# Performance work log

Measured on AMD Instinct MI355X. Metric: run time of the kernel, lower is better.

## Reference

```python
import math
import jax, jax.numpy as jnp
import numpy as np

B, L, D, H = 2, 2048, 1024, 16
HD = D // H  # 64

def setup_inputs() -> dict:
    key = jax.random.key(0)
    k1, k2, k3 = jax.random.split(key, 3)
    x = jax.random.normal(k1, (B, L, D), dtype=jnp.float32)
    Wqkv = jax.random.normal(k2, (3 * D, D), dtype=jnp.float32) * (1.0 / math.sqrt(D))
    Wo = jax.random.normal(k3, (D, D), dtype=jnp.float32) * (1.0 / math.sqrt(D))
    return {"x": x, "Wqkv": Wqkv, "Wo": Wo}

def reference(x, Wqkv, Wo):
    # QKV projection (torch Linear: y = x @ W.T), then split
    qkv = jnp.einsum('bld,ed->ble', x, Wqkv)  # [B, L, 3D]
    q, k, v = jnp.split(qkv, 3, axis=-1)
    # [B, H, L, HD]
    q = q.reshape(B, L, H, HD).transpose(0, 2, 1, 3)
    k = k.reshape(B, L, H, HD).transpose(0, 2, 1, 3)
    v = v.reshape(B, L, H, HD).transpose(0, 2, 1, 3)
    # scores; causal mask applied before the 1/sqrt(d) scale (as in source;
    # -inf is unchanged by scaling so math matches scale-then-mask)
    scores = jnp.einsum('bhqd,bhkd->bhqk', q, k)
    causal = jnp.tril(jnp.ones((L, L), dtype=bool))
    scores = jnp.where(causal, scores, -jnp.inf)
    attn = jax.nn.softmax(scores / math.sqrt(HD), axis=-1)
    out = jnp.einsum('bhqk,bhkd->bhqd', attn, v)  # [B, H, L, HD]
    out = out.transpose(0, 2, 1, 3).reshape(B, L, D)
    # output projection (dropout is identity in eval / p=0)
    return jnp.einsum('bld,ed->ble', out, Wo)
```

## Files before the change

### kernel.cpp

```cpp
#include <hip/hip_runtime.h>
#include <hip/hip_bf16.h>
#include <cstdint>
#include <cstddef>

#define B_SZ 2
#define L_SEQ 2048
#define DM 1024
#define NH 16
#define HDIM 64
#define BL (B_SZ * L_SEQ)
#define QKV_N (3 * DM)

typedef __attribute__((ext_vector_type(4))) float f32x4;
typedef __attribute__((ext_vector_type(16))) float f32x16;
typedef __attribute__((ext_vector_type(8))) short bf16x8;
typedef __attribute__((ext_vector_type(4))) unsigned int u32x4;
typedef unsigned short u16;
typedef __attribute__((ext_vector_type(4))) unsigned short u16x4;

__device__ __forceinline__ float bf2f(u16 u) {
  union { unsigned int i; float f; } c; c.i = ((unsigned int)u) << 16; return c.f;
}
__device__ __forceinline__ u16 f2bf(float f) {
  union { float f; unsigned int i; } c; c.f = f;
  unsigned int r = c.i + 0x7fffu + ((c.i >> 16) & 1u);
  return (u16)(r >> 16);
}

__device__ __forceinline__ void gload_lds16(const void* g, void* l) {
  __builtin_amdgcn_global_load_lds(
      (const __attribute__((address_space(1))) void*)g,
      (__attribute__((address_space(3))) void*)l, 16, 0, 0);
}

__device__ __forceinline__ f32x16 mfma32(bf16x8 a, bf16x8 b, f32x16 c) {
  return __builtin_amdgcn_mfma_f32_32x32x16_bf16(a, b, c, 0, 0, 0);
}

__device__ __forceinline__ unsigned cvtpk(float lo, float hi) {
  unsigned r;
  asm("v_cvt_pk_bf16_f32 %0, %1, %2" : "=v"(r) : "v"(lo), "v"(hi));
  return r;
}
__device__ __forceinline__ void plswap(unsigned& a, unsigned& b) {
  asm("v_permlane32_swap_b32 %0, %1" : "+v"(a), "+v"(b));
}

template <int BASE>
__device__ __forceinline__ bf16x8 pack_bfrag(const f32x16& v) {
  unsigned a  = cvtpk(v[BASE + 0], v[BASE + 1]);
  unsigned a2 = cvtpk(v[BASE + 2], v[BASE + 3]);
  unsigned b  = cvtpk(v[BASE + 4], v[BASE + 5]);
  unsigned b2 = cvtpk(v[BASE + 6], v[BASE + 7]);
  plswap(a, b);
  plswap(a2, b2);
  u32x4 fw; fw[0] = a; fw[1] = a2; fw[2] = b; fw[3] = b2;
  return __builtin_bit_cast(bf16x8, fw);
}

__global__ __launch_bounds__(256) void cvt_f32_bf16(const float* __restrict__ in,
                                                    u16* __restrict__ out, int n4) {
  int i = blockIdx.x * blockDim.x + threadIdx.x;
  const int stride = gridDim.x * blockDim.x;
  for (; i < n4; i += stride) {
    float4 v = ((const float4*)in)[i];
    u16x4 o;
    o[0] = f2bf(v.x); o[1] = f2bf(v.y); o[2] = f2bf(v.z); o[3] = f2bf(v.w);
    ((u16x4*)out)[i] = o;
  }
}

template <bool BF16_OUT>
__global__ __launch_bounds__(256) void gemm_bt(
    const u16* __restrict__ A, const u16* __restrict__ B,
    void* __restrict__ Cv, int M, int N, int K) {
  __shared__ u16 As[128 * 32];
  __shared__ u16 Bs[128 * 32];
  const int tid = threadIdx.x;
  const int lane = tid & 63, w = tid >> 6;
  const int lr = lane & 15, lg = lane >> 4;
  const int wr = w >> 1, wc = w & 1;
  const int bm = blockIdx.y * 128, bn = blockIdx.x * 128;

  f32x4 acc[4][4] = {};

  const int l4 = lane >> 2;
  const int csw = ((lane & 3) ^ ((lane >> 3) & 3)) * 8;
  const size_t aoff0 = (size_t)(bm + (w * 2 + 0) * 16 + l4) * K + csw;
  const size_t aoff1 = (size_t)(bm + (w * 2 + 1) * 16 + l4) * K + csw;
  const size_t boff0 = (size_t)(bn + (w * 2 + 0) * 16 + l4) * K + csw;
  const size_t boff1 = (size_t)(bn + (w * 2 + 1) * 16 + l4) * K + csw;
  u16* As0 = As + (w * 2 + 0) * 512;
  u16* As1 = As + (w * 2 + 1) * 512;
  u16* Bs0 = Bs + (w * 2 + 0) * 512;
  u16* Bs1 = Bs + (w * 2 + 1) * 512;
  const int sw_rd = (lr >> 1) & 3;

  for (int k0 = 0; k0 < K; k0 += 32) {
    gload_lds16(A + aoff0 + k0, As0);
    gload_lds16(A + aoff1 + k0, As1);
    gload_lds16(B + boff0 + k0, Bs0);
    gload_lds16(B + boff1 + k0, Bs1);
    __syncthreads();

    bf16x8 af[4], bfr[4];
#pragma unroll
    for (int mt = 0; mt < 4; ++mt) {
      const int row = wr * 64 + mt * 16 + lr;
      af[mt] = *(const bf16x8*)&As[row * 32 + ((lg ^ sw_rd) * 8)];
    }
#pragma unroll
    for (int nt = 0; nt < 4; ++nt) {
      const int row = wc * 64 + nt * 16 + lr;
      bfr[nt] = *(const bf16x8*)&Bs[row * 32 + ((lg ^ sw_rd) * 8)];
    }
#pragma unroll
    for (int mt = 0; mt < 4; ++mt)
#pragma unroll
      for (int nt = 0; nt < 4; ++nt)
        acc[mt][nt] = __builtin_amdgcn_mfma_f32_16x16x32_bf16(af[mt], bfr[nt],
                                                              acc[mt][nt], 0, 0, 0);
    __syncthreads();
  }

#pragma unroll
  for (int mt = 0; mt < 4; ++mt)
#pragma unroll
    for (int nt = 0; nt < 4; ++nt)
#pragma unroll
      for (int r = 0; r < 4; ++r) {
        const int row = bm + wr * 64 + mt * 16 + lg * 4 + r;
        const int col = bn + wc * 64 + nt * 16 + lr;
        if (BF16_OUT)
          ((u16*)Cv)[(size_t)row * N + col] = f2bf(acc[mt][nt][r]);
        else
          ((float*)Cv)[(size_t)row * N + col] = acc[mt][nt][r];
      }
}

__device__ const uint8_t JQT[24] = {15,14,13,12,11,10,9,8, 7, 15, 14,6, 13,5,
                                    12,4, 11,3, 10,2, 9,1, 8,0};
__device__ const uint8_t JT0[24] = {0,0,0,0,0,0,0,0, 0, 16, 16,0, 16,0,
                                    16,0, 16,0, 16,0, 16,0, 16,0};
__device__ const uint8_t JT1[24] = {16,16,16,16,16,16,16,16, 16, 32, 30,14, 28,12,
                                    26,10, 24,8, 22,6, 20,4, 18,2};

__global__ __launch_bounds__(256) void attn_fused(const u16* __restrict__ qkv,
                                                  u16* __restrict__ aout,
                                                  float* __restrict__ opart,
                                                  float2* __restrict__ mlb) {
  __shared__ u16 Kl[2][64 * 64];
  __shared__ u16 Vt[2][64 * 64];

  const int tid = threadIdx.x;
  const int lane = tid & 63, w = tid >> 6;
  const int l31 = lane & 31, hi = lane >> 5;
  const int id = (int)blockIdx.x;
  const int bh = id & 31, j = id >> 5;
  const int qt = JQT[j];
  const int t0 = JT0[j], t1 = JT1[j];
  const int b = bh >> 4, h = bh & 15;
  const u16* base = qkv + (size_t)b * L_SEQ * QKV_N;
  const int W = qt * 128 + w * 32;
  const int qrow = W + l31;

  const int krow = tid >> 2;
  const int ks0 = (tid & 3) * 2;
  const int kr7 = krow & 7;
  const u16* gpk_base = base + (size_t)krow * QKV_N + DM + h * HDIM + ks0 * 8;
  bf16x8 kr0, kr1;

  const int vd0 = (tid & 31) * 2;
  const int vkb = tid >> 5;
  const int vge = tid & 7;
  const int vgo = (tid & 7) ^ 4;
  const u16* gpv_base = base + (size_t)(vkb * 8) * QKV_N + 2 * DM + h * HDIM + vd0;
  unsigned int vtmp[8];

  auto issue_loads = [&](int t) {
    const u16* gpk = gpk_base + (size_t)t * 64 * QKV_N;
    kr0 = *(const bf16x8*)(gpk);
    kr1 = *(const bf16x8*)(gpk + 8);
    const u16* gpv = gpv_base + (size_t)t * 64 * QKV_N;
#pragma unroll
    for (int jj = 0; jj < 8; ++jj)
      vtmp[jj] = *(const unsigned int*)(gpv + (size_t)jj * QKV_N);
  };
  auto write_lds = [&](int buf) {
    *(bf16x8*)&Kl[buf][krow * 64 + ((ks0 ^ kr7) * 8)] = kr0;
    *(bf16x8*)&Kl[buf][krow * 64 + (((ks0 + 1) ^ kr7) * 8)] = kr1;
    u32x4 lo, hiw;
#pragma unroll
    for (int jj = 0; jj < 4; ++jj) {
      lo[jj]  = __builtin_amdgcn_perm(vtmp[2 * jj + 1], vtmp[2 * jj], 0x05040100u);
      hiw[jj] = __builtin_amdgcn_perm(vtmp[2 * jj + 1], vtmp[2 * jj], 0x07060302u);
    }
    *(u32x4*)&Vt[buf][vd0 * 64 + ((vkb ^ vge) * 8)] = lo;
    *(u32x4*)&Vt[buf][(vd0 + 1) * 64 + ((vkb ^ vgo) * 8)] = hiw;
  };

  bf16x8 bq[4];
  {
    const u16* qp = base + (size_t)qrow * QKV_N + h * HDIM + hi * 8;
#pragma unroll
    for (int dc = 0; dc < 4; ++dc) {
      bf16x8 tq = *(const bf16x8*)(qp + dc * 16);
#pragma unroll
      for (int i = 0; i < 8; ++i)
        tq[i] = (short)f2bf(bf2f((u16)tq[i]) * 0.18033688f);
      bq[dc] = tq;
    }
  }

  f32x16 acc0 = {}, acc1 = {};
  float mrow = -1e30f, lrow = 0.f;

  const int vg = ((l31 >> 1) & 7) ^ ((l31 & 1) << 2);
  const int lsw = l31 & 7;

  issue_loads(t0);
  write_lds(0);
  __syncthreads();

  for (int t = t0; t < t1; ++t) {
    const int cur = (t - t0) & 1;
    if (t + 1 < t1) issue_loads(t + 1);

    if (64 * t <= W + 31) {
      f32x16 s0 = {}, s1 = {};
#pragma unroll
      for (int dc = 0; dc < 4; ++dc) {
        const int sl = ((dc * 2 + hi) ^ lsw) * 8;
        const bf16x8 k0 = *(const bf16x8*)&Kl[cur][l31 * 64 + sl];
        const bf16x8 k1 = *(const bf16x8*)&Kl[cur][(32 + l31) * 64 + sl];
        s0 = mfma32(k0, bq[dc], s0);
        s1 = mfma32(k1, bq[dc], s1);
      }

      if (64 * t + 63 > W) {
#pragma unroll
        for (int r = 0; r < 16; ++r) {
          const int kg = t * 64 + (r & 3) + 8 * (r >> 2) + 4 * hi;
          if (kg > qrow) s0[r] = -1e30f;
          if (kg + 32 > qrow) s1[r] = -1e30f;
        }
      }

      float mx[8];
#pragma unroll
      for (int i = 0; i < 8; ++i)
        mx[i] = fmaxf(fmaxf(s0[i], s0[i + 8]), fmaxf(s1[i], s1[i + 8]));
#pragma unroll
      for (int i = 0; i < 4; ++i) mx[i] = fmaxf(mx[i], mx[i + 4]);
      float px = fmaxf(fmaxf(mx[0], mx[2]), fmaxf(mx[1], mx[3]));
      px = fmaxf(px, __shfl_xor(px, 32));

      if (!__all(px <= mrow + 8.f)) {
        const float mnew = fmaxf(mrow, px);
        const float alpha = exp2f(mrow - mnew);
        mrow = mnew;
        lrow *= alpha;
#pragma unroll
        for (int i = 0; i < 16; ++i) { acc0[i] *= alpha; acc1[i] *= alpha; }
      }

#pragma unroll
      for (int r = 0; r < 16; ++r) {
        s0[r] = exp2f(s0[r] - mrow);
        s1[r] = exp2f(s1[r] - mrow);
      }
      float sm[8];
#pragma unroll
      for (int i = 0; i < 8; ++i)
        sm[i] = (s0[i] + s0[i + 8]) + (s1[i] + s1[i + 8]);
#pragma unroll
      for (int i = 0; i < 4; ++i) sm[i] += sm[i + 4];
      float rs = (sm[0] + sm[2]) + (sm[1] + sm[3]);
      rs += __shfl_xor(rs, 32);
      lrow += rs;

      const bf16x8 pf0 = pack_bfrag<0>(s0);
      const bf16x8 pf1 = pack_bfrag<8>(s0);
      const bf16x8 pf2 = pack_bfrag<0>(s1);
      const bf16x8 pf3 = pack_bfrag<8>(s1);

#pragma unroll
      for (int c = 0; c < 4; ++c) {
        const bf16x8 pf = c == 0 ? pf0 : c == 1 ? pf1 : c == 2 ? pf2 : pf3;
        const int sl = ((c * 2 + hi) ^ vg) * 8;
        const bf16x8 va = *(const bf16x8*)&Vt[cur][l31 * 64 + sl];
        const bf16x8 vb = *(const bf16x8*)&Vt[cur][(32 + l31) * 64 + sl];
        acc0 = mfma32(va, pf, acc0);
        acc1 = mfma32(vb, pf, acc1);
      }
    }

    if (t + 1 < t1) write_lds(((t + 1) - t0) & 1);
    __syncthreads();
  }

  if (qt >= 8) {
    const int c = (t0 == 16) ? 1 : 0;
    const int slot = ((qt - 8) * 2 + c) * 32 + bh;
    float* po = opart + (size_t)slot * 8192 + (w * 32 + l31);
#pragma unroll
    for (int i = 0; i < 16; ++i) {
      const int d0 = (i & 3) + 8 * (i >> 2) + 4 * hi;
      po[d0 * 128] = acc0[i];
      po[(d0 + 32) * 128] = acc1[i];
    }
    if (hi == 0) mlb[slot * 128 + w * 32 + l31] = make_float2(mrow, lrow);
  } else {
    const float inv = 1.f / lrow;
#pragma unroll
    for (int i = 0; i < 16; ++i) { acc0[i] *= inv; acc1[i] *= inv; }
    const bf16x8 of0 = pack_bfrag<0>(acc0);
    const bf16x8 of1 = pack_bfrag<8>(acc0);
    const bf16x8 of2 = pack_bfrag<0>(acc1);
    const bf16x8 of3 = pack_bfrag<8>(acc1);
    u16* op = aout + (size_t)(b * L_SEQ + qrow) * DM + h * HDIM + hi * 8;
    *(bf16x8*)(op + 0)  = of0;
    *(bf16x8*)(op + 16) = of1;
    *(bf16x8*)(op + 32) = of2;
    *(bf16x8*)(op + 48) = of3;
  }
}

__global__ __launch_bounds__(256) void attn_combine(
    const float* __restrict__ opart, const float2* __restrict__ mlb,
    u16* __restrict__ aout) {
  const int gw = ((int)blockIdx.x * 256 + (int)threadIdx.x) >> 6;
  const int lane = threadIdx.x & 63;
  const int u = gw >> 1, qh = gw & 1;
  const int qt = 8 + (u >> 5), bh = u & 31;
  const int b = bh >> 4, h = bh & 15;
  const int s1 = ((qt - 8) * 2) * 32 + bh, s2 = s1 + 32;
  const int q = qh * 64 + lane;
  const float2 ml1 = mlb[s1 * 128 + q];
  const float2 ml2 = mlb[s2 * 128 + q];
  const float m = fmaxf(ml1.x, ml2.x);
  const float a1 = exp2f(ml1.x - m), a2 = exp2f(ml2.x - m);
  const float invl = 1.f / (ml1.y * a1 + ml2.y * a2);
  const float c1 = a1 * invl, c2 = a2 * invl;
  const float* p1 = opart + (size_t)s1 * 8192 + q;
  const float* p2 = opart + (size_t)s2 * 8192 + q;
  const int qrow = qt * 128 + q;
  u16* op = aout + (size_t)(b * L_SEQ + qrow) * DM + h * HDIM;
#pragma unroll
  for (int d0 = 0; d0 < 64; d0 += 8) {
    u16x4 o0, o1;
#pragma unroll
    for (int jj = 0; jj < 4; ++jj) {
      o0[jj] = f2bf(p1[(d0 + jj) * 128] * c1 + p2[(d0 + jj) * 128] * c2);
      o1[jj] = f2bf(p1[(d0 + 4 + jj) * 128] * c1 + p2[(d0 + 4 + jj) * 128] * c2);
    }
    *(u16x4*)(op + d0) = o0;
    *(u16x4*)(op + d0 + 4) = o1;
  }
}

extern "C" void kernel_launch(void* const* d_in, const int* in_sizes, int n_in,
                              void* d_out, int out_size, void* d_ws, size_t ws_size,
                              hipStream_t stream) {
  (void)in_sizes; (void)n_in; (void)out_size; (void)ws_size;
  const float* x = (const float*)d_in[0];
  const float* wqkv = (const float*)d_in[1];
  const float* wo = (const float*)d_in[2];

  char* ws = (char*)d_ws;
  u16* x_bf = (u16*)(ws);
  u16* w_bf = (u16*)(ws + (size_t)(8u << 20));
  u16* wo_bf = (u16*)(ws + (size_t)(14u << 20));
  u16* qkv_bf = (u16*)(ws + (size_t)(16u << 20));
  u16* ao_bf = x_bf;
  float* opart = (float*)d_out;
  float2* mlb = (float2*)(ws + (size_t)(8u << 20));

  cvt_f32_bf16<<<2048, 256, 0, stream>>>(x, x_bf, BL * DM / 4);
  cvt_f32_bf16<<<2048, 256, 0, stream>>>(wqkv, w_bf, QKV_N * DM / 4);
  cvt_f32_bf16<<<1024, 256, 0, stream>>>(wo, wo_bf, DM * DM / 4);

  dim3 g1(QKV_N / 128, BL / 128);
  gemm_bt<true><<<g1, 256, 0, stream>>>(x_bf, w_bf, (void*)qkv_bf, BL, QKV_N, DM);

  attn_fused<<<dim3(768), 256, 0, stream>>>(qkv_bf, ao_bf, opart, mlb);
  attn_combine<<<dim3(128), 256, 0, stream>>>(opart, mlb, ao_bf);

  dim3 g3(DM / 128, BL / 128);
  gemm_bt<false><<<g3, 256, 0, stream>>>(ao_bf, wo_bf, d_out, BL, DM, DM);
}
```

Measured before the change: 138.6 us.

## Split causal attention KV range into finer chunks with bf16 partials

Reworks the causal attention work split so that query tiles 4-15 are divided into KV chunks of 8 tiles (up to 4 chunks per query tile). This grows the grid from 768 to 1280 blocks for better load balance across CUs. Partial outputs are now stored as bf16 instead of fp32, spread over two buffers, to cut partial-result traffic. The combine kernel now merges up to four partials per row. The cost is more combine work, a larger split-KV overhead, and slightly lower precision in the partials.

```diff
diff --git a/kernel.cpp b/kernel.cpp
--- a/kernel.cpp
+++ b/kernel.cpp
@@ -138,16 +138,22 @@
       }
 }
 
-__device__ const uint8_t JQT[24] = {15,14,13,12,11,10,9,8, 7, 15, 14,6, 13,5,
-                                    12,4, 11,3, 10,2, 9,1, 8,0};
-__device__ const uint8_t JT0[24] = {0,0,0,0,0,0,0,0, 0, 16, 16,0, 16,0,
-                                    16,0, 16,0, 16,0, 16,0, 16,0};
-__device__ const uint8_t JT1[24] = {16,16,16,16,16,16,16,16, 16, 32, 30,14, 28,12,
-                                    26,10, 24,8, 22,6, 20,4, 18,2};
+__device__ const uint8_t JQT[40] = {15,15,15,15, 14,14,14, 13,13,13, 12,12,12,
+                                    11,11,11, 10,10, 9,9, 8,8, 7,7, 6, 5, 4, 3,
+                                    14, 10, 6, 2, 13, 9, 5, 1, 12, 8, 4, 0};
+__device__ const uint8_t JT0[40] = {0,8,16,24, 0,8,16, 0,8,16, 0,8,16,
+                                    0,8,16, 0,8, 0,8, 0,8, 0,8, 0, 0, 0, 0,
+                                    24, 16, 8, 0, 24, 16, 8, 0, 24, 16, 8, 0};
+__device__ const uint8_t JT1[40] = {8,16,24,32, 8,16,24, 8,16,24, 8,16,24,
+                                    8,16,24, 8,16, 8,16, 8,16, 8,16, 8, 8, 8, 8,
+                                    30, 22, 14, 6, 28, 20, 12, 4, 26, 18, 10, 2};
+__device__ const uint8_t SBASE[16] = {255,255,255,255, 0,2,4,6,
+                                      8,11,14,17, 20,24,28,32};
 
 __global__ __launch_bounds__(256) void attn_fused(const u16* __restrict__ qkv,
                                                   u16* __restrict__ aout,
-                                                  float* __restrict__ opart,
+                                                  u16* __restrict__ opart_lo,
+                                                  u16* __restrict__ opart_hi,
                                                   float2* __restrict__ mlb) {
   __shared__ u16 Kl[2][64 * 64];
   __shared__ u16 Vt[2][64 * 64];
@@ -299,17 +305,19 @@
     __syncthreads();
   }
 
-  if (qt >= 8) {
-    const int c = (t0 == 16) ? 1 : 0;
-    const int slot = ((qt - 8) * 2 + c) * 32 + bh;
-    float* po = opart + (size_t)slot * 8192 + (w * 32 + l31);
+  if (SBASE[qt] != 255) {
+    const int c = t0 >> 3;
+    const int slot = ((int)SBASE[qt] + c) * 32 + bh;
+    u16* po = slot < 1024 ? opart_lo + (size_t)slot * 8192
+                          : opart_hi + (size_t)(slot - 1024) * 8192;
+    const int q = w * 32 + l31;
 #pragma unroll
     for (int i = 0; i < 16; ++i) {
       const int d0 = (i & 3) + 8 * (i >> 2) + 4 * hi;
-      po[d0 * 128] = acc0[i];
-      po[(d0 + 32) * 128] = acc1[i];
-    }
-    if (hi == 0) mlb[slot * 128 + w * 32 + l31] = make_float2(mrow, lrow);
+      po[d0 * 128 + q] = f2bf(acc0[i]);
+      po[(d0 + 32) * 128 + q] = f2bf(acc1[i]);
+    }
+    if (hi == 0) mlb[slot * 128 + q] = make_float2(mrow, lrow);
   } else {
     const float inv = 1.f / lrow;
 #pragma unroll
@@ -327,35 +335,54 @@
 }
 
 __global__ __launch_bounds__(256) void attn_combine(
-    const float* __restrict__ opart, const float2* __restrict__ mlb,
-    u16* __restrict__ aout) {
-  const int gw = ((int)blockIdx.x * 256 + (int)threadIdx.x) >> 6;
-  const int lane = threadIdx.x & 63;
-  const int u = gw >> 1, qh = gw & 1;
-  const int qt = 8 + (u >> 5), bh = u & 31;
+    const u16* __restrict__ opart_lo, const u16* __restrict__ opart_hi,
+    const float2* __restrict__ mlb, u16* __restrict__ aout) {
+  const int gid = (int)blockIdx.x * 256 + (int)threadIdx.x;
+  const int q = gid & 127;
+  const int u = gid >> 7;
+  const int qt = 4 + (u >> 5), bh = u & 31;
   const int b = bh >> 4, h = bh & 15;
-  const int s1 = ((qt - 8) * 2) * 32 + bh, s2 = s1 + 32;
-  const int q = qh * 64 + lane;
-  const float2 ml1 = mlb[s1 * 128 + q];
-  const float2 ml2 = mlb[s2 * 128 + q];
-  const float m = fmaxf(ml1.x, ml2.x);
-  const float a1 = exp2f(ml1.x - m), a2 = exp2f(ml2.x - m);
-  const float invl = 1.f / (ml1.y * a1 + ml2.y * a2);
-  const float c1 = a1 * invl, c2 = a2 * invl;
-  const float* p1 = opart + (size_t)s1 * 8192 + q;
-  const float* p2 = opart + (size_t)s2 * 8192 + q;
+  const int nc = (2 * qt + 9) >> 3;
+  const int sb = (int)SBASE[qt];
+
+  float2 ml[4];
+  const u16* pp[4];
+  float mm = -1e30f;
+#pragma unroll
+  for (int c = 0; c < 4; ++c)
+    if (c < nc) {
+      const int slot = (sb + c) * 32 + bh;
+      ml[c] = mlb[slot * 128 + q];
+      pp[c] = slot < 1024 ? opart_lo + (size_t)slot * 8192
+                          : opart_hi + (size_t)(slot - 1024) * 8192;
+      mm = fmaxf(mm, ml[c].x);
+    }
+  float L = 0.f, cf[4];
+#pragma unroll
+  for (int c = 0; c < 4; ++c)
+    if (c < nc) { cf[c] = exp2f(ml[c].x - mm); L += ml[c].y * cf[c]; }
+  const float invl = 1.f / L;
+#pragma unroll
+  for (int c = 0; c < 4; ++c)
+    if (c < nc) cf[c] *= invl;
+
   const int qrow = qt * 128 + q;
   u16* op = aout + (size_t)(b * L_SEQ + qrow) * DM + h * HDIM;
 #pragma unroll
   for (int d0 = 0; d0 < 64; d0 += 8) {
-    u16x4 o0, o1;
-#pragma unroll
-    for (int jj = 0; jj < 4; ++jj) {
-      o0[jj] = f2bf(p1[(d0 + jj) * 128] * c1 + p2[(d0 + jj) * 128] * c2);
-      o1[jj] = f2bf(p1[(d0 + 4 + jj) * 128] * c1 + p2[(d0 + 4 + jj) * 128] * c2);
-    }
-    *(u16x4*)(op + d0) = o0;
-    *(u16x4*)(op + d0 + 4) = o1;
+    float v[8] = {};
+#pragma unroll
+    for (int c = 0; c < 4; ++c)
+      if (c < nc) {
+#pragma unroll
+        for (int jj = 0; jj < 8; ++jj)
+          v[jj] += cf[c] * bf2f(pp[c][(d0 + jj) * 128 + q]);
+      }
+    u16x4 oa, ob;
+#pragma unroll
+    for (int jj = 0; jj < 4; ++jj) { oa[jj] = f2bf(v[jj]); ob[jj] = f2bf(v[jj + 4]); }
+    *(u16x4*)(op + d0) = oa;
+    *(u16x4*)(op + d0 + 4) = ob;
   }
 }
 
@@ -373,8 +400,9 @@
   u16* wo_bf = (u16*)(ws + (size_t)(14u << 20));
   u16* qkv_bf = (u16*)(ws + (size_t)(16u << 20));
   u16* ao_bf = x_bf;
-  float* opart = (float*)d_out;
-  float2* mlb = (float2*)(ws + (size_t)(8u << 20));
+  u16* opart_lo = (u16*)d_out;
+  u16* opart_hi = (u16*)(ws + (size_t)(8u << 20));
+  float2* mlb = (float2*)(ws + (size_t)(10u << 20));
 
   cvt_f32_bf16<<<2048, 256, 0, stream>>>(x, x_bf, BL * DM / 4);
   cvt_f32_bf16<<<2048, 256, 0, stream>>>(wqkv, w_bf, QKV_N * DM / 4);
@@ -383,8 +411,8 @@
   dim3 g1(QKV_N / 128, BL / 128);
   gemm_bt<true><<<g1, 256, 0, stream>>>(x_bf, w_bf, (void*)qkv_bf, BL, QKV_N, DM);
 
-  attn_fused<<<dim3(768), 256, 0, stream>>>(qkv_bf, ao_bf, opart, mlb);
-  attn_combine<<<dim3(128), 256, 0, stream>>>(opart, mlb, ao_bf);
+  attn_fused<<<dim3(1280), 256, 0, stream>>>(qkv_bf, ao_bf, opart_lo, opart_hi, mlb);
+  attn_combine<<<dim3(192), 256, 0, stream>>>(opart_lo, opart_hi, mlb, ao_bf);
 
   dim3 g3(DM / 128, BL / 128);
   gemm_bt<false><<<g3, 256, 0, stream>>>(ao_bf, wo_bf, d_out, BL, DM, DM);
```

After: 143.6 us. +3.6%, slower.
